# Optimization experiments

Hardware: AMD Instinct MI355X
Metric: run time of the kernel (lower is better)

The kernel has to match this reference:

```python
import jax, jax.numpy as jnp
import numpy as np

# ConvMem dims
B, Cx, Cy, L, K, S, N = 64, 16, 64, 32, 5, 1, 1024
M = (L - K) // S + 1  # 28
DT, TAU_X, TAU_Y = 0.1, 1.0, 0.1
ETA_X, ETA_Y = DT / TAU_X, DT / TAU_Y
MAX_STEPS = 50


def setup_inputs() -> dict:
    key = jax.random.key(0)
    k1, k2, k3, k4 = jax.random.split(key, 4)
    x0 = jax.random.normal(k1, (B, Cx, L, L), dtype=jnp.float32)
    f0 = jax.random.uniform(k2, (B, Cy, M, M), dtype=jnp.float32) / 100.0
    # Conv2d weight (shared between conv and convT), shape (Cy, Cx, K, K)
    w_conv = jax.random.normal(k3, (Cy, Cx, K, K), dtype=jnp.float32) / np.sqrt(Cx * K * K).astype(np.float32)
    # W: (N, Cy*M*M), kaiming_normal fan_in init
    W = jax.random.normal(k4, (N, Cy * M * M), dtype=jnp.float32) * np.sqrt(2.0 / (Cy * M * M)).astype(np.float32)
    return {"x0": x0, "f0": f0, "w_conv": w_conv, "W": W}


def _conv(x, w):
    # PyTorch Conv2d(Cx, Cy, K, S, bias=False), valid padding
    return jax.lax.conv_general_dilated(x, w, (S, S), 'VALID',
                                        dimension_numbers=('NCHW', 'OIHW', 'NCHW'))


def _convT(f, w):
    # PyTorch ConvTranspose2d with the *same* weight as conv (adjoint of _conv)
    return jax.lax.conv_transpose(f, w, (S, S), 'VALID',
                                  dimension_numbers=('NCHW', 'OIHW', 'NCHW'),
                                  transpose_kernel=True)


def reference(x0, f0, w_conv, W):
    def step(carry, _):
        x_prev, f_prev = carry
        # fc: z = W @ flatten(f_prev);  g = softmax(z) over N (dim=1, beta=1)
        z = jnp.einsum('nk,bk->bn', W, f_prev.reshape(B, Cy * M * M))  # (B, N)
        g = jax.nn.softmax(z, axis=1)
        # fcT: y = W^T @ g, reshaped to (B, Cy, M, M)
        y = (g @ W).reshape(B, Cy, M, M)
        # f nonlin: softmax over channel dim (dim=1)
        f_new = jax.nn.softmax(y + _conv(x_prev, w_conv), axis=1)
        x_new = _convT(f_prev, w_conv)
        f = (1.0 - ETA_Y) * f_prev + ETA_Y * f_new
        x = (1.0 - ETA_X) * x_prev + ETA_X * x_new
        return (x, f), None

    (x, f), _ = jax.lax.scan(step, (x0, f0), None, length=MAX_STEPS)
    return x, f
```

## Files before the change

kernel.cpp:

```cpp
#include <hip/hip_runtime.h>

#define BB 64
#define CXC 16
#define CYC 64
#define LL 32
#define MM 28
#define NN 1024
#define SP 784
#define KTOT 50176
#define NSTEPS 50
#define NSPLIT 49

using short8  = __attribute__((ext_vector_type(8))) short;
using floatx4 = __attribute__((ext_vector_type(4))) float;

typedef __attribute__((address_space(1))) unsigned int gu32;
typedef __attribute__((address_space(3))) unsigned int su32;

__device__ __forceinline__ ushort f2b(float v) {
    union { float f; unsigned u; } a; a.f = v;
    unsigned r = a.u + 0x7fff + ((a.u >> 16) & 1);
    return (ushort)(r >> 16);
}
__device__ __forceinline__ unsigned pk2(float a, float b) {
    return (unsigned)f2b(a) | ((unsigned)f2b(b) << 16);
}
__device__ __forceinline__ float b2f(ushort u) {
    union { unsigned u; float f; } a; a.u = ((unsigned)u) << 16; return a.f;
}

__device__ __forceinline__ unsigned char f2e4(float v) {
    const unsigned u = __float_as_uint(v);
    const unsigned s = (u >> 24) & 0x80;
    float a = fabsf(v);
    if (a >= 448.f) return (unsigned char)(s | 0x7E);
    if (a < 0.015625f) {
        int q = (int)rintf(a * 512.f);
        return (unsigned char)(s | (unsigned)q);
    }
    unsigned au = u & 0x7fffffffu;
    unsigned r = au + 0xFFFFFu + ((au >> 20) & 1u);
    int exp = (int)(r >> 23) - 127;
    if (exp > 8) return (unsigned char)(s | 0x7E);
    unsigned mant = (r >> 20) & 7u;
    return (unsigned char)(s | (((unsigned)(exp + 7)) << 3) | mant);
}

__device__ __forceinline__ unsigned pk4e4(float a, float b, float c, float d) {
#if __has_builtin(__builtin_amdgcn_cvt_pk_fp8_f32)
    unsigned u = 0;
    u = __builtin_amdgcn_cvt_pk_fp8_f32(a, b, u, false);
    u = __builtin_amdgcn_cvt_pk_fp8_f32(c, d, u, true);
    return u;
#else
    return (unsigned)f2e4(a) | ((unsigned)f2e4(b) << 8)
         | ((unsigned)f2e4(c) << 16) | ((unsigned)f2e4(d) << 24);
#endif
}

#define WSC 256.0f
#define FSC 64.0f
#define GSC 256.0f
#define ZDESC (1.0f / (WSC * FSC))
#define YDESC (1.0f / (WSC * GSC))

__global__ __launch_bounds__(256) void wconvert_kernel(const float* __restrict__ W,
                                                       unsigned char* __restrict__ Wb8,
                                                       unsigned char* __restrict__ WT8) {
    __shared__ float t[64 * 68];
    const int k0 = blockIdx.x * 64, n0 = blockIdx.y * 64;
    const int tid = threadIdx.x;
    for (int c = tid; c < 1024; c += 256) {
        const int row = c >> 4, col4 = (c & 15) * 4;
        const float4 v = *(const float4*)(W + (size_t)(n0 + row) * KTOT + k0 + col4);
        *(float4*)&t[row * 68 + col4] = v;
    }
    __syncthreads();
    const int rr = tid >> 2, cb = (tid & 3) * 16;
    {
        uint4 o;
        const float* p = &t[rr * 68 + cb];
        o.x = pk4e4(p[0] * WSC,  p[1] * WSC,  p[2] * WSC,  p[3] * WSC);
        o.y = pk4e4(p[4] * WSC,  p[5] * WSC,  p[6] * WSC,  p[7] * WSC);
        o.z = pk4e4(p[8] * WSC,  p[9] * WSC,  p[10] * WSC, p[11] * WSC);
        o.w = pk4e4(p[12] * WSC, p[13] * WSC, p[14] * WSC, p[15] * WSC);
        *(uint4*)&Wb8[(size_t)(n0 + rr) * KTOT + k0 + cb] = o;
    }
    {
        uint4 o;
        const float* p = &t[cb * 68 + rr];
        o.x = pk4e4(p[0*68] * WSC,  p[1*68] * WSC,  p[2*68] * WSC,  p[3*68] * WSC);
        o.y = pk4e4(p[4*68] * WSC,  p[5*68] * WSC,  p[6*68] * WSC,  p[7*68] * WSC);
        o.z = pk4e4(p[8*68] * WSC,  p[9*68] * WSC,  p[10*68] * WSC, p[11*68] * WSC);
        o.w = pk4e4(p[12*68] * WSC, p[13*68] * WSC, p[14*68] * WSC, p[15*68] * WSC);
        *(uint4*)&WT8[(size_t)(k0 + rr) * NN + n0 + cb] = o;
    }
}

__global__ __launch_bounds__(256) void cvt_f0_kernel(const float* __restrict__ f,
                                                     unsigned char* __restrict__ o) {
    const size_t i = ((size_t)blockIdx.x * 256 + threadIdx.x) * 4;
    const float4 v = *(const float4*)(f + i);
    uchar4 pk;
    pk.x = f2e4(v.x * FSC); pk.y = f2e4(v.y * FSC);
    pk.z = f2e4(v.z * FSC); pk.w = f2e4(v.w * FSC);
    *(uchar4*)(o + i) = pk;
}

__global__ __launch_bounds__(256) void wbuild_kernel(const float* __restrict__ wc,
                                                     ushort* __restrict__ wcA,
                                                     ushort* __restrict__ wcT) {
    const int bid = blockIdx.x, tid = threadIdx.x;
    if (bid < 64) {
        const int cy = bid;
        for (int k = tid; k < 416; k += 256) {
            const int tap = k >> 4, cx = k & 15;
            const float v = (tap < 25) ? wc[cy * 400 + cx * 25 + tap] : 0.f;
            wcA[cy * 416 + k] = f2b(v);
        }
    } else {
        const int cx = bid - 64;
        for (int k = tid; k < 1600; k += 256) {
            const int tap = k >> 6, cy = k & 63;
            wcT[cx * 1600 + k] = f2b(wc[cy * 400 + cx * 25 + tap]);
        }
    }
}

__global__ __launch_bounds__(256) void init_x_kernel(const float* __restrict__ x0,
                                                     float* __restrict__ xcl,
                                                     ushort* __restrict__ x16) {
    const int b = blockIdx.x, tid = threadIdx.x;
    __shared__ float xs[16384];
    for (int c = tid; c < 4096; c += 256)
        ((float4*)xs)[c] = ((const float4*)(x0 + (size_t)b * 16384))[c];
    __syncthreads();
    for (int p = tid; p < 1024; p += 256) {
        float v[16];
#pragma unroll
        for (int cx = 0; cx < 16; cx++) v[cx] = xs[cx * 1024 + p];
        float* dst = xcl + ((size_t)b * 1024 + p) * 16;
#pragma unroll
        for (int q = 0; q < 4; q++)
            *(float4*)(dst + q * 4) = make_float4(v[q*4], v[q*4+1], v[q*4+2], v[q*4+3]);
        uint4 u0, u1;
        u0.x = pk2(v[0], v[1]);  u0.y = pk2(v[2], v[3]);
        u0.z = pk2(v[4], v[5]);  u0.w = pk2(v[6], v[7]);
        u1.x = pk2(v[8], v[9]);  u1.y = pk2(v[10], v[11]);
        u1.z = pk2(v[12], v[13]); u1.w = pk2(v[14], v[15]);
        ushort* d16 = x16 + ((size_t)b * 1024 + p) * 16;
        *(uint4*)d16 = u0; *(uint4*)(d16 + 8) = u1;
    }
}

__global__ __launch_bounds__(256) void final_x_kernel(const float* __restrict__ xcl,
                                                      float* __restrict__ dout) {
    const int b = blockIdx.x, tid = threadIdx.x;
    __shared__ float xs[16384];
    for (int c = tid; c < 4096; c += 256)
        ((float4*)xs)[c] = ((const float4*)(xcl + (size_t)b * 16384))[c];
    __syncthreads();
    for (int idx = tid; idx < 16384; idx += 256) {
        const int cx = idx >> 10, p = idx & 1023;
        dout[(size_t)b * 16384 + idx] = xs[p * 16 + cx];
    }
}

__global__ __launch_bounds__(256) void init_fpad_kernel(const float* __restrict__ f0,
                                                        ushort* __restrict__ fpad) {
    const int b = blockIdx.x, rg = blockIdx.y;
    const int tid = threadIdx.x;
    __shared__ float fs[64 * 112];
    const float* src = f0 + (size_t)b * KTOT + rg * 112;
    for (int c = tid; c < 1792; c += 256) {
        const int cy = c / 28, p4 = (c % 28) * 4;
        *(float4*)&fs[cy * 112 + p4] = *(const float4*)(src + (size_t)cy * SP + p4);
    }
    __syncthreads();
    for (int c = tid; c < 896; c += 256) {
        const int pl = c >> 3, g8 = (c & 7) * 8;
        union { ushort u[8]; uint4 v; } pk;
#pragma unroll
        for (int e = 0; e < 8; e++) pk.u[e] = f2b(fs[(g8 + e) * 112 + pl]);
        const int pos = rg * 112 + pl, i = pos / 28, j = pos % 28;
        *(uint4*)(fpad + (((size_t)b * 36 + 4 + i) * 36 + 4 + j) * 64 + g8) = pk.v;
    }
}

__global__ __launch_bounds__(256, 3) void gemm1_kernel(const unsigned char* __restrict__ A,
                                                       const unsigned char* __restrict__ B,
                                                       float* __restrict__ C) {
    const int bx = blockIdx.x, by = blockIdx.y;
    const int tid = threadIdx.x, l = tid & 63, w = tid >> 6;
    const int wr = w >> 1, wc = w & 1;
    const int lr = l & 15, lg = l >> 4;
    const int sw = (lr >> 1) & 3;
    const int hi8 = (lg & 1) * 8;
    __shared__ __attribute__((aligned(16))) unsigned char As[3 * 4096];
    __shared__ __attribute__((aligned(16))) unsigned char Bs[3 * 8192];

    floatx4 acc[2][4];
#pragma unroll
    for (int mi = 0; mi < 2; mi++)
#pragma unroll
        for (int ni = 0; ni < 4; ni++) acc[mi][ni] = (floatx4){0.f, 0.f, 0.f, 0.f};

    const size_t kbase = (size_t)by * 1024;

    auto STAGE = [&](int buf, int kc) {
        const size_t koff = kbase + (size_t)kc * 64;
        {
            const int row = tid >> 2;
            const int kk = (((tid & 3) ^ ((row >> 1) & 3)) << 4);
            __builtin_amdgcn_global_load_lds((gu32*)(A + (size_t)row * KTOT + koff + kk),
                                             (su32*)&As[buf * 4096 + tid * 16], 16, 0, 0);
        }
#pragma unroll
        for (int i = 0; i < 2; i++) {
            const int q = i * 256 + tid;
            const int rl = q >> 2;
            const int kk = (((q & 3) ^ ((rl >> 1) & 3)) << 4);
            const int row = bx * 128 + rl;
            __builtin_amdgcn_global_load_lds((gu32*)(B + (size_t)row * KTOT + koff + kk),
                                             (su32*)&Bs[buf * 8192 + q * 16], 16, 0, 0);
        }
    };

    STAGE(0, 0);
    int cur = 0;
#pragma unroll 1
    for (int kc = 0; kc < 16; kc++) {
        if (kc < 15) {
            int nb = cur + 1; if (nb == 3) nb = 0;
            STAGE(nb, kc + 1);
            asm volatile("s_waitcnt vmcnt(3)" ::: "memory");
        } else {
            asm volatile("s_waitcnt vmcnt(0)" ::: "memory");
        }
        __builtin_amdgcn_s_barrier();
#pragma unroll
        for (int kb = 0; kb < 2; kb++) {
            const int co = (((kb * 2 + (lg >> 1)) ^ sw) << 4) + hi8;
            long a[2];
#pragma unroll
            for (int mi = 0; mi < 2; mi++)
                a[mi] = *(const long*)&As[cur * 4096 + (wr * 32 + mi * 16 + lr) * 64 + co];
#pragma unroll
            for (int ni = 0; ni < 4; ni++) {
                const long b = *(const long*)&Bs[cur * 8192 + (wc * 64 + ni * 16 + lr) * 64 + co];
                acc[0][ni] = __builtin_amdgcn_mfma_f32_16x16x32_fp8_fp8(a[0], b, acc[0][ni], 0, 0, 0);
                acc[1][ni] = __builtin_amdgcn_mfma_f32_16x16x32_fp8_fp8(a[1], b, acc[1][ni], 0, 0, 0);
            }
        }
        cur = cur + 1; if (cur == 3) cur = 0;
    }
    float* cp = C + (size_t)by * (BB * NN) + (size_t)(wr * 32 + ((l >> 4) << 2)) * NN
              + bx * 128 + wc * 64 + (l & 15);
#pragma unroll
    for (int mi = 0; mi < 2; mi++)
#pragma unroll
        for (int ni = 0; ni < 4; ni++)
#pragma unroll
            for (int q = 0; q < 4; q++)
                cp[(size_t)(mi * 16 + q) * NN + ni * 16] = acc[mi][ni][q];
}

__global__ __launch_bounds__(1024) void softmax_g_kernel(const float* __restrict__ zpart,
                                                         unsigned char* __restrict__ g8) {
    const int b = blockIdx.x, tid = threadIdx.x;
    float s = 0.f;
#pragma unroll 7
    for (int sp = 0; sp < NSPLIT; sp++) s += zpart[(size_t)sp * (BB * NN) + b * NN + tid];
    s *= ZDESC;
    __shared__ float red[32];
    float m = s;
#pragma unroll
    for (int off = 32; off > 0; off >>= 1) m = fmaxf(m, __shfl_down(m, off));
    if ((tid & 63) == 0) red[tid >> 6] = m;
    __syncthreads();
    float bm = red[0];
#pragma unroll
    for (int e = 1; e < 16; e++) bm = fmaxf(bm, red[e]);
    const float ev = __expf(s - bm);
    float ssum = ev;
#pragma unroll
    for (int off = 32; off > 0; off >>= 1) ssum += __shfl_down(ssum, off);
    __syncthreads();
    if ((tid & 63) == 0) red[16 + (tid >> 6)] = ssum;
    __syncthreads();
    float tot = red[16];
#pragma unroll
    for (int e = 1; e < 16; e++) tot += red[16 + e];
    g8[b * NN + tid] = f2e4(ev * (GSC / tot));
}

__global__ __launch_bounds__(256, 3) void gemm2_convT_kernel(const unsigned char* __restrict__ A,
                                                             const unsigned char* __restrict__ B,
                                                             float* __restrict__ C,
                                                             const ushort* __restrict__ fpad,
                                                             const ushort* __restrict__ wcT,
                                                             const float* __restrict__ xin,
                                                             float* __restrict__ xout,
                                                             ushort* __restrict__ x16o) {
    __shared__ __attribute__((aligned(16))) unsigned char As[3 * 4096];
    __shared__ __attribute__((aligned(16))) unsigned char Bs[3 * 8192];
    const int tid = threadIdx.x, l = tid & 63, w = tid >> 6;
    const int lr = l & 15, lg = l >> 4;

    if (blockIdx.x < 256) {
        const int sub = blockIdx.x, b = sub & 63, pg = sub >> 6;
        floatx4 acc[4];
#pragma unroll
        for (int n = 0; n < 4; n++) acc[n] = (floatx4){0.f, 0.f, 0.f, 0.f};
        int p[4], p1[4], p2[4];
#pragma unroll
        for (int n = 0; n < 4; n++) {
            p[n]  = pg * 256 + (w * 4 + n) * 16 + lr;
            p1[n] = p[n] >> 5;
            p2[n] = p[n] & 31;
        }
        const ushort* fb_b = fpad + (size_t)b * (36 * 36 * 64);
        const int cy_lo = lg * 8;

        for (int s = 0; s < 50; s++) {
            const short8 af = *(const short8*)(wcT + (size_t)lr * 1600 + s * 32 + lg * 8);
            const int tap = s >> 1;
            const int ky = tap / 5, kx = tap % 5;
            const int cy_lane = ((s & 1) << 5) + cy_lo;
            short8 bf[4];
#pragma unroll
            for (int n = 0; n < 4; n++) {
                const size_t ad = (((size_t)(p1[n] + 4 - ky)) * 36 + (p2[n] + 4 - kx)) * 64 + cy_lane;
                bf[n] = *(const short8*)(fb_b + ad);
            }
#pragma unroll
            for (int n = 0; n < 4; n++)
                acc[n] = __builtin_amdgcn_mfma_f32_16x16x32_bf16(af, bf[n], acc[n], 0, 0, 0);
        }
#pragma unroll
        for (int n = 0; n < 4; n++) {
            const size_t base = ((size_t)b * 1024 + p[n]) * 16 + lg * 4;
            const float4 xo = *(const float4*)(xin + base);
            float4 r;
            r.x = 0.9f * xo.x + 0.1f * acc[n][0];
            r.y = 0.9f * xo.y + 0.1f * acc[n][1];
            r.z = 0.9f * xo.z + 0.1f * acc[n][2];
            r.w = 0.9f * xo.w + 0.1f * acc[n][3];
            *(float4*)(xout + base) = r;
            uint2 pk; pk.x = pk2(r.x, r.y); pk.y = pk2(r.z, r.w);
            *(uint2*)(x16o + base) = pk;
        }
        return;
    }

    const int bx = blockIdx.x - 256;
    const int wr = w >> 1, wc = w & 1;
    const int sw = (lr >> 1) & 3;
    const int hi8 = (lg & 1) * 8;

    floatx4 acc[2][4];
#pragma unroll
    for (int mi = 0; mi < 2; mi++)
#pragma unroll
        for (int ni = 0; ni < 4; ni++) acc[mi][ni] = (floatx4){0.f, 0.f, 0.f, 0.f};

    auto STAGE = [&](int buf, int kc) {
        const size_t koff = (size_t)kc * 64;
        {
            const int row = tid >> 2;
            const int kk = (((tid & 3) ^ ((row >> 1) & 3)) << 4);
            __builtin_amdgcn_global_load_lds((gu32*)(A + (size_t)row * NN + koff + kk),
                                             (su32*)&As[buf * 4096 + tid * 16], 16, 0, 0);
        }
#pragma unroll
        for (int i = 0; i < 2; i++) {
            const int q = i * 256 + tid;
            const int rl = q >> 2;
            const int kk = (((q & 3) ^ ((rl >> 1) & 3)) << 4);
            const int row = bx * 128 + rl;
            __builtin_amdgcn_global_load_lds((gu32*)(B + (size_t)row * NN + koff + kk),
                                             (su32*)&Bs[buf * 8192 + q * 16], 16, 0, 0);
        }
    };

    STAGE(0, 0);
    int cur = 0;
#pragma unroll 1
    for (int kc = 0; kc < 16; kc++) {
        if (kc < 15) {
            int nb = cur + 1; if (nb == 3) nb = 0;
            STAGE(nb, kc + 1);
            asm volatile("s_waitcnt vmcnt(3)" ::: "memory");
        } else {
            asm volatile("s_waitcnt vmcnt(0)" ::: "memory");
        }
        __builtin_amdgcn_s_barrier();
#pragma unroll
        for (int kb = 0; kb < 2; kb++) {
            const int co = (((kb * 2 + (lg >> 1)) ^ sw) << 4) + hi8;
            long a[2];
#pragma unroll
            for (int mi = 0; mi < 2; mi++)
                a[mi] = *(const long*)&As[cur * 4096 + (wr * 32 + mi * 16 + lr) * 64 + co];
#pragma unroll
            for (int ni = 0; ni < 4; ni++) {
                const long b = *(const long*)&Bs[cur * 8192 + (wc * 64 + ni * 16 + lr) * 64 + co];
                acc[0][ni] = __builtin_amdgcn_mfma_f32_16x16x32_fp8_fp8(a[0], b, acc[0][ni], 0, 0, 0);
                acc[1][ni] = __builtin_amdgcn_mfma_f32_16x16x32_fp8_fp8(a[1], b, acc[1][ni], 0, 0, 0);
            }
        }
        cur = cur + 1; if (cur == 3) cur = 0;
    }
    float* cp = C + (size_t)(wr * 32 + ((l >> 4) << 2)) * KTOT
              + bx * 128 + wc * 64 + (l & 15);
#pragma unroll
    for (int mi = 0; mi < 2; mi++)
#pragma unroll
        for (int ni = 0; ni < 4; ni++)
#pragma unroll
            for (int q = 0; q < 4; q++)
                cp[(size_t)(mi * 16 + q) * KTOT + ni * 16] = acc[mi][ni][q];
}

__global__ __launch_bounds__(256) void conv_mfma_kernel(const ushort* __restrict__ x16,
                                                        const ushort* __restrict__ wcA,
                                                        const float* __restrict__ y,
                                                        ushort* __restrict__ fpad,
                                                        unsigned char* __restrict__ f8std,
                                                        float* __restrict__ f32o,
                                                        const int write_f) {
    const int b = blockIdx.x, rg = blockIdx.y;
    const int tid = threadIdx.x, l = tid & 63, w = tid >> 6;
    const int lr = l & 15, lg = l >> 4;
    __shared__ float yt[64 * 196];
    ushort* ft = (ushort*)yt;

    {
        const float* yb = y + (size_t)b * KTOT + rg * 196;
        for (int c = tid; c < 3136; c += 256) {
            const int cy = c / 49, p4 = (c % 49) * 4;
            float4 v = *(const float4*)(yb + (size_t)cy * SP + p4);
            v.x *= YDESC; v.y *= YDESC; v.z *= YDESC; v.w *= YDESC;
            *(float4*)&yt[cy * 196 + p4] = v;
        }
    }

    const int nf = (w == 0) ? 4 : 3;
    const int fb = (w == 0) ? 0 : (1 + 3 * w);

    floatx4 acc[4][4];
#pragma unroll
    for (int m = 0; m < 4; m++)
#pragma unroll
        for (int n = 0; n < 4; n++) acc[m][n] = (floatx4){0.f, 0.f, 0.f, 0.f};

    int pos_l[4], ii[4], jj[4];
#pragma unroll
    for (int n = 0; n < 4; n++) {
        int pl = (fb + n) * 16 + lr;
        if (pl > 195) pl = 195;
        pos_l[n] = pl;
        ii[n] = rg * 7 + pl / 28;
        jj[n] = pl % 28;
    }

    const int t_lane = lg >> 1;
    const int cx0 = (lg & 1) * 8;
    const ushort* xb = x16 + ((size_t)b << 14);

    for (int s = 0; s < 13; s++) {
        short8 af[4];
#pragma unroll
        for (int m = 0; m < 4; m++)
            af[m] = *(const short8*)(wcA + (size_t)(m * 16 + lr) * 416 + s * 32 + lg * 8);
        const int tap = 2 * s + t_lane;
        const int ky = tap / 5, kx = tap % 5;
        short8 bf[4];
#pragma unroll
        for (int n = 0; n < 4; n++) {
            if (n < nf) {
                const int pp = (ii[n] + ky) * 32 + (jj[n] + kx);
                bf[n] = *(const short8*)(xb + (size_t)pp * 16 + cx0);
            }
        }
#pragma unroll
        for (int n = 0; n < 4; n++) {
            if (n < nf) {
#pragma unroll
                for (int m = 0; m < 4; m++)
                    acc[m][n] = __builtin_amdgcn_mfma_f32_16x16x32_bf16(af[m], bf[n], acc[m][n], 0, 0, 0);
            }
        }
    }
    __syncthreads();

#pragma unroll
    for (int n = 0; n < 4; n++) {
        if (n < nf) {
            float v[16];
#pragma unroll
            for (int m = 0; m < 4; m++)
#pragma unroll
                for (int q = 0; q < 4; q++) {
                    const int cy = m * 16 + lg * 4 + q;
                    v[m * 4 + q] = acc[m][n][q] + yt[cy * 196 + pos_l[n]];
                }
            float mx = v[0];
#pragma unroll
            for (int e = 1; e < 16; e++) mx = fmaxf(mx, v[e]);
            mx = fmaxf(mx, __shfl_xor(mx, 16));
            mx = fmaxf(mx, __shfl_xor(mx, 32));
            float ss = 0.f;
#pragma unroll
            for (int e = 0; e < 16; e++) { v[e] = __expf(v[e] - mx); ss += v[e]; }
            ss += __shfl_xor(ss, 16);
            ss += __shfl_xor(ss, 32);
            const float inv = 1.0f / ss;
            const bool valid = (((fb + n) * 16 + lr) < 196) && write_f;
            float* fo = f32o + (size_t)b * KTOT + rg * 196 + pos_l[n];
#pragma unroll
            for (int m = 0; m < 4; m++)
#pragma unroll
                for (int q = 0; q < 4; q++) {
                    const int cy = m * 16 + lg * 4 + q;
                    const float fv = v[m * 4 + q] * inv;
                    acc[m][n][q] = fv;
                    if (valid) fo[(size_t)cy * SP] = fv;
                }
        }
    }
    __syncthreads();

#pragma unroll
    for (int n = 0; n < 4; n++) {
        if (n < nf) {
#pragma unroll
            for (int m = 0; m < 4; m++)
#pragma unroll
                for (int q = 0; q < 4; q++)
                    ft[pos_l[n] * 72 + m * 16 + lg * 4 + q] = f2b(acc[m][n][q]);
        }
    }
    __syncthreads();

    for (int c = tid; c < 196 * 4; c += 256) {
        const int pl = c >> 2, ch = (c & 3) * 16;
        const uint4 v0 = *(const uint4*)&ft[pl * 72 + ch];
        const uint4 v1 = *(const uint4*)&ft[pl * 72 + ch + 8];
        const int gi = rg * 7 + pl / 28, gj = pl % 28;
        ushort* dst = fpad + (((size_t)b * 36 + 4 + gi) * 36 + 4 + gj) * 64 + ch;
        *(uint4*)dst = v0; *(uint4*)(dst + 8) = v1;
    }
    for (int c = tid; c < 1600; c += 256) {
        const int cy = c & 63, p8 = (c >> 6) * 8;
        if (p8 < 196) {
            union { unsigned char u[8]; unsigned w[2]; } pk;
#pragma unroll
            for (int e = 0; e < 8; e++)
                pk.u[e] = f2e4(b2f(ft[(p8 + e) * 72 + cy]) * FSC);
            unsigned* dst = (unsigned*)(f8std + (size_t)b * KTOT + (size_t)cy * SP + rg * 196 + p8);
            dst[0] = pk.w[0];
            if (p8 <= 188) dst[1] = pk.w[1];
        }
    }
}

extern "C" void kernel_launch(void* const* d_in, const int* in_sizes, int n_in,
                              void* d_out, int out_size, void* d_ws, size_t ws_size,
                              hipStream_t stream) {
    const float* x0    = (const float*)d_in[0];
    const float* f0    = (const float*)d_in[1];
    const float* wconv = (const float*)d_in[2];
    const float* W     = (const float*)d_in[3];

    const size_t XSZ = (size_t)BB * CXC * LL * LL;
    const size_t FSZ = (size_t)BB * KTOT;

    char* pp = (char*)d_ws;
    unsigned char* Wb8  = (unsigned char*)pp; pp += (size_t)NN * KTOT;
    unsigned char* WT8  = (unsigned char*)pp; pp += (size_t)NN * KTOT;
    float*  xcl0  = (float*)pp;  pp += (size_t)BB * 1024 * 16 * 4;
    float*  xcl1  = (float*)pp;  pp += (size_t)BB * 1024 * 16 * 4;
    ushort* x16a  = (ushort*)pp; pp += (size_t)BB * 1024 * 16 * 2;
    ushort* x16b  = (ushort*)pp; pp += (size_t)BB * 1024 * 16 * 2;
    pp += 4096;
    ushort* fpad  = (ushort*)pp; pp += (size_t)BB * 36 * 36 * 64 * 2;
    unsigned char* f8std = (unsigned char*)pp; pp += FSZ;
    float*  zy    = (float*)pp;  pp += (size_t)NSPLIT * BB * NN * 4;
    unsigned char* g8 = (unsigned char*)pp; pp += (size_t)BB * NN;
    ushort* wcA   = (ushort*)pp; pp += (size_t)64 * 416 * 2;
    ushort* wcT   = (ushort*)pp; pp += (size_t)16 * 1600 * 2;

    float*  xcl[2] = {xcl0, xcl1};
    ushort* x16[2] = {x16a, x16b};
    float*  f32o = (float*)d_out + XSZ;

    hipMemsetAsync(fpad, 0, (size_t)BB * 36 * 36 * 64 * 2, stream);
    hipMemsetAsync(x16a, 0, (size_t)BB * 1024 * 16 * 2 * 2 + 4096, stream);

    wconvert_kernel<<<dim3(KTOT / 64, NN / 64), 256, 0, stream>>>(W, Wb8, WT8);
    wbuild_kernel<<<80, 256, 0, stream>>>(wconv, wcA, wcT);
    init_x_kernel<<<64, 256, 0, stream>>>(x0, xcl0, x16a);
    cvt_f0_kernel<<<(int)(FSZ / 1024), 256, 0, stream>>>(f0, f8std);
    init_fpad_kernel<<<dim3(64, 7), 256, 0, stream>>>(f0, fpad);

    for (int t = 0; t < NSTEPS; t++) {
        const int cur = t & 1, nxt = cur ^ 1;
        gemm1_kernel<<<dim3(8, NSPLIT), 256, 0, stream>>>(f8std, Wb8, zy);
        softmax_g_kernel<<<BB, 1024, 0, stream>>>(zy, g8);
        gemm2_convT_kernel<<<256 + KTOT / 128, 256, 0, stream>>>(
            g8, WT8, zy, fpad, wcT, xcl[cur], xcl[nxt], x16[nxt]);
        conv_mfma_kernel<<<dim3(64, 4), 256, 0, stream>>>(x16[cur], wcA, zy, fpad, f8std, f32o,
                                                          t == NSTEPS - 1 ? 1 : 0);
    }
    final_x_kernel<<<64, 256, 0, stream>>>(xcl[0], (float*)d_out);
}
```

Baseline: 4.275 ms.

## Fuse split-K reduction and softmax into gemm1 via int atomics; store y as bf16

The split-K partial results of the first GEMM are now accumulated with fixed-point integer atomics into one buffer instead of being written as 49 float partial slabs. The last block to finish, found through a global counter, computes the row softmax and writes the fp8 g, so the separate softmax kernel launch goes away. The second GEMM now writes y as pre-scaled bf16 instead of fp32, halving the traffic read by the conv kernel. In exchange this adds atomic contention, a fixed-point rounding error, and a serial softmax tail done by a single block with only four threads per row.

```diff
diff --git a/kernel.cpp b/kernel.cpp
--- a/kernel.cpp
+++ b/kernel.cpp
@@ -63,6 +63,8 @@
 #define GSC 256.0f
 #define ZDESC (1.0f / (WSC * FSC))
 #define YDESC (1.0f / (WSC * GSC))
+#define ZQ 1024.0f
+#define ZS (1.0f / (16384.0f * 1024.0f))
 
 __global__ __launch_bounds__(256) void wconvert_kernel(const float* __restrict__ W,
                                                        unsigned char* __restrict__ Wb8,
@@ -98,8 +100,18 @@
 }
 
 __global__ __launch_bounds__(256) void cvt_f0_kernel(const float* __restrict__ f,
-                                                     unsigned char* __restrict__ o) {
-    const size_t i = ((size_t)blockIdx.x * 256 + threadIdx.x) * 4;
+                                                     unsigned char* __restrict__ o,
+                                                     int* __restrict__ z_int,
+                                                     unsigned* __restrict__ cnt) {
+    const int bid = blockIdx.x, tid = threadIdx.x;
+    if (bid < 64) {
+        int* zi = z_int + bid * 1024 + tid * 4;
+        atomicExch(&zi[0], 0); atomicExch(&zi[1], 0);
+        atomicExch(&zi[2], 0); atomicExch(&zi[3], 0);
+    } else if (bid == 64 && tid < NSTEPS) {
+        atomicExch(&cnt[tid], 0u);
+    }
+    const size_t i = ((size_t)bid * 256 + tid) * 4;
     const float4 v = *(const float4*)(f + i);
     uchar4 pk;
     pk.x = f2e4(v.x * FSC); pk.y = f2e4(v.y * FSC);
@@ -189,7 +201,10 @@
 
 __global__ __launch_bounds__(256, 3) void gemm1_kernel(const unsigned char* __restrict__ A,
                                                        const unsigned char* __restrict__ B,
-                                                       float* __restrict__ C) {
+                                                       int* __restrict__ z_int,
+                                                       float* __restrict__ zscr,
+                                                       unsigned char* __restrict__ g8,
+                                                       unsigned* __restrict__ cnt) {
     const int bx = blockIdx.x, by = blockIdx.y;
     const int tid = threadIdx.x, l = tid & 63, w = tid >> 6;
     const int wr = w >> 1, wc = w & 1;
@@ -254,49 +269,60 @@
         }
         cur = cur + 1; if (cur == 3) cur = 0;
     }
-    float* cp = C + (size_t)by * (BB * NN) + (size_t)(wr * 32 + ((l >> 4) << 2)) * NN
-              + bx * 128 + wc * 64 + (l & 15);
+    int* zp = z_int + (wr * 32 + ((l >> 4) << 2)) * NN + bx * 128 + wc * 64 + (l & 15);
 #pragma unroll
     for (int mi = 0; mi < 2; mi++)
 #pragma unroll
         for (int ni = 0; ni < 4; ni++)
 #pragma unroll
             for (int q = 0; q < 4; q++)
-                cp[(size_t)(mi * 16 + q) * NN + ni * 16] = acc[mi][ni][q];
-}
-
-__global__ __launch_bounds__(1024) void softmax_g_kernel(const float* __restrict__ zpart,
-                                                         unsigned char* __restrict__ g8) {
-    const int b = blockIdx.x, tid = threadIdx.x;
-    float s = 0.f;
-#pragma unroll 7
-    for (int sp = 0; sp < NSPLIT; sp++) s += zpart[(size_t)sp * (BB * NN) + b * NN + tid];
-    s *= ZDESC;
-    __shared__ float red[32];
-    float m = s;
-#pragma unroll
-    for (int off = 32; off > 0; off >>= 1) m = fmaxf(m, __shfl_down(m, off));
-    if ((tid & 63) == 0) red[tid >> 6] = m;
-    __syncthreads();
-    float bm = red[0];
-#pragma unroll
-    for (int e = 1; e < 16; e++) bm = fmaxf(bm, red[e]);
-    const float ev = __expf(s - bm);
-    float ssum = ev;
-#pragma unroll
-    for (int off = 32; off > 0; off >>= 1) ssum += __shfl_down(ssum, off);
-    __syncthreads();
-    if ((tid & 63) == 0) red[16 + (tid >> 6)] = ssum;
-    __syncthreads();
-    float tot = red[16];
-#pragma unroll
-    for (int e = 1; e < 16; e++) tot += red[16 + e];
-    g8[b * NN + tid] = f2e4(ev * (GSC / tot));
+                atomicAdd(&zp[(mi * 16 + q) * NN + ni * 16],
+                          (int)rintf(acc[mi][ni][q] * ZQ));
+
+    __threadfence();
+    __syncthreads();
+    __shared__ unsigned lastf;
+    if (tid == 0) lastf = (atomicAdd(cnt, 1u) == (unsigned)(8 * NSPLIT - 1)) ? 1u : 0u;
+    __syncthreads();
+    if (lastf == 0u) return;
+    __threadfence();
+
+    const int r = tid >> 2, seg = tid & 3;
+    float* scr = zscr + r * 1024;
+    int* zi = z_int + r * 1024;
+    float mx = -1e30f;
+#pragma unroll 4
+    for (int i = 0; i < 256; i++) {
+        const int n = i * 4 + seg;
+        const int v = atomicExch(&zi[n], 0);
+        const float zf = (float)v * ZS;
+        scr[n] = zf;
+        mx = fmaxf(mx, zf);
+    }
+    mx = fmaxf(mx, __shfl_xor(mx, 1));
+    mx = fmaxf(mx, __shfl_xor(mx, 2));
+    float ssum = 0.f;
+#pragma unroll 4
+    for (int i = 0; i < 256; i++) {
+        const int n = i * 4 + seg;
+        const float e = __expf(scr[n] - mx);
+        scr[n] = e;
+        ssum += e;
+    }
+    ssum += __shfl_xor(ssum, 1);
+    ssum += __shfl_xor(ssum, 2);
+    const float gsc = GSC / ssum;
+    unsigned char* gout = g8 + r * 1024;
+#pragma unroll 4
+    for (int i = 0; i < 256; i++) {
+        const int n = i * 4 + seg;
+        gout[n] = f2e4(scr[n] * gsc);
+    }
 }
 
 __global__ __launch_bounds__(256, 3) void gemm2_convT_kernel(const unsigned char* __restrict__ A,
                                                              const unsigned char* __restrict__ B,
-                                                             float* __restrict__ C,
+                                                             ushort* __restrict__ y8,
                                                              const ushort* __restrict__ fpad,
                                                              const ushort* __restrict__ wcT,
                                                              const float* __restrict__ xin,
@@ -411,20 +437,20 @@
         }
         cur = cur + 1; if (cur == 3) cur = 0;
     }
-    float* cp = C + (size_t)(wr * 32 + ((l >> 4) << 2)) * KTOT
-              + bx * 128 + wc * 64 + (l & 15);
+    ushort* cp = y8 + (size_t)(wr * 32 + ((l >> 4) << 2)) * KTOT
+               + bx * 128 + wc * 64 + (l & 15);
 #pragma unroll
     for (int mi = 0; mi < 2; mi++)
 #pragma unroll
         for (int ni = 0; ni < 4; ni++)
 #pragma unroll
             for (int q = 0; q < 4; q++)
-                cp[(size_t)(mi * 16 + q) * KTOT + ni * 16] = acc[mi][ni][q];
+                cp[(size_t)(mi * 16 + q) * KTOT + ni * 16] = f2b(acc[mi][ni][q] * YDESC);
 }
 
 __global__ __launch_bounds__(256) void conv_mfma_kernel(const ushort* __restrict__ x16,
                                                         const ushort* __restrict__ wcA,
-                                                        const float* __restrict__ y,
+                                                        const ushort* __restrict__ y8,
                                                         ushort* __restrict__ fpad,
                                                         unsigned char* __restrict__ f8std,
                                                         float* __restrict__ f32o,
@@ -436,12 +462,14 @@
     ushort* ft = (ushort*)yt;
 
     {
-        const float* yb = y + (size_t)b * KTOT + rg * 196;
+        const ushort* yb = y8 + (size_t)b * KTOT + rg * 196;
         for (int c = tid; c < 3136; c += 256) {
             const int cy = c / 49, p4 = (c % 49) * 4;
-            float4 v = *(const float4*)(yb + (size_t)cy * SP + p4);
-            v.x *= YDESC; v.y *= YDESC; v.z *= YDESC; v.w *= YDESC;
-            *(float4*)&yt[cy * 196 + p4] = v;
+            const uint2 u = *(const uint2*)(yb + (size_t)cy * SP + p4);
+            yt[cy * 196 + p4 + 0] = b2f((ushort)(u.x & 0xffff));
+            yt[cy * 196 + p4 + 1] = b2f((ushort)(u.x >> 16));
+            yt[cy * 196 + p4 + 2] = b2f((ushort)(u.y & 0xffff));
+            yt[cy * 196 + p4 + 3] = b2f((ushort)(u.y >> 16));
         }
     }
 
@@ -586,8 +614,11 @@
     pp += 4096;
     ushort* fpad  = (ushort*)pp; pp += (size_t)BB * 36 * 36 * 64 * 2;
     unsigned char* f8std = (unsigned char*)pp; pp += FSZ;
-    float*  zy    = (float*)pp;  pp += (size_t)NSPLIT * BB * NN * 4;
+    ushort* y8    = (ushort*)pp; pp += FSZ * 2;
     unsigned char* g8 = (unsigned char*)pp; pp += (size_t)BB * NN;
+    int*    z_int = (int*)pp;    pp += (size_t)BB * NN * 4;
+    float*  zscr  = (float*)pp;  pp += (size_t)BB * NN * 4;
+    unsigned* cnt = (unsigned*)pp; pp += 4096;
     ushort* wcA   = (ushort*)pp; pp += (size_t)64 * 416 * 2;
     ushort* wcT   = (ushort*)pp; pp += (size_t)16 * 1600 * 2;
 
@@ -601,16 +632,15 @@
     wconvert_kernel<<<dim3(KTOT / 64, NN / 64), 256, 0, stream>>>(W, Wb8, WT8);
     wbuild_kernel<<<80, 256, 0, stream>>>(wconv, wcA, wcT);
     init_x_kernel<<<64, 256, 0, stream>>>(x0, xcl0, x16a);
-    cvt_f0_kernel<<<(int)(FSZ / 1024), 256, 0, stream>>>(f0, f8std);
+    cvt_f0_kernel<<<(int)(FSZ / 1024), 256, 0, stream>>>(f0, f8std, z_int, cnt);
     init_fpad_kernel<<<dim3(64, 7), 256, 0, stream>>>(f0, fpad);
 
     for (int t = 0; t < NSTEPS; t++) {
         const int cur = t & 1, nxt = cur ^ 1;
-        gemm1_kernel<<<dim3(8, NSPLIT), 256, 0, stream>>>(f8std, Wb8, zy);
-        softmax_g_kernel<<<BB, 1024, 0, stream>>>(zy, g8);
+        gemm1_kernel<<<dim3(8, NSPLIT), 256, 0, stream>>>(f8std, Wb8, z_int, zscr, g8, cnt + t);
         gemm2_convT_kernel<<<256 + KTOT / 128, 256, 0, stream>>>(
-            g8, WT8, zy, fpad, wcT, xcl[cur], xcl[nxt], x16[nxt]);
-        conv_mfma_kernel<<<dim3(64, 4), 256, 0, stream>>>(x16[cur], wcA, zy, fpad, f8std, f32o,
+            g8, WT8, y8, fpad, wcT, xcl[cur], xcl[nxt], x16[nxt]);
+        conv_mfma_kernel<<<dim3(64, 4), 256, 0, stream>>>(x16[cur], wcA, y8, fpad, f8std, f32o,
                                                           t == NSTEPS - 1 ? 1 : 0);
     }
     final_x_kernel<<<64, 256, 0, stream>>>(xcl[0], (float*)d_out);
```

After: 12.30 ms. 2.88x slower.
